# Performance work log

Measured on AMD Instinct MI355X. Metric: run time of the kernel, lower is better.

Reference implementation:

```python
import jax, jax.numpy as jnp
import numpy as np

N_NODES = 100000
N_EDGES = 1600000
VOCAB = 50000
EMB = 128
HID = 128
N_CLASSES = 10
N_GRAPHS = 512


def gcn_conv(x, src, dst, W, b, n_nodes):
    # PyG GCNConv: add self-loops, symmetric normalization D^-1/2 (A+I) D^-1/2, then linear.
    h = x @ W  # [N, H]
    loop = jnp.arange(n_nodes)
    s = jnp.concatenate([src, loop])
    d = jnp.concatenate([dst, loop])
    deg = jax.ops.segment_sum(jnp.ones_like(d, dtype=h.dtype), d, num_segments=n_nodes)
    dinv = jnp.where(deg > 0, jax.lax.rsqrt(deg), 0.0)
    norm = dinv[s] * dinv[d]  # [E+N]
    msg = h[s] * norm[:, None]  # gather + scale
    out = jax.ops.segment_sum(msg, d, num_segments=n_nodes)  # scatter-add
    return out + b


def setup_inputs() -> dict:
    key = jax.random.key(0)
    ks = jax.random.split(key, 10)
    x_idx = jax.random.randint(ks[0], (N_NODES,), 0, VOCAB)
    edge_index = jax.random.randint(ks[1], (2, N_EDGES), 0, N_NODES)
    batch = jnp.sort(jax.random.randint(ks[2], (N_NODES,), 0, N_GRAPHS))
    emb = jax.random.normal(ks[3], (VOCAB, EMB), dtype=jnp.float32)
    W1 = jax.random.normal(ks[4], (EMB, HID), dtype=jnp.float32) / np.sqrt(EMB)
    b1 = jnp.zeros((HID,), dtype=jnp.float32)
    W2 = jax.random.normal(ks[5], (HID, HID), dtype=jnp.float32) / np.sqrt(HID)
    b2 = jnp.zeros((HID,), dtype=jnp.float32)
    linW = jax.random.normal(ks[6], (HID, N_CLASSES), dtype=jnp.float32) / np.sqrt(HID)
    linb = jnp.zeros((N_CLASSES,), dtype=jnp.float32)
    return {"x_idx": x_idx, "edge_index": edge_index, "batch": batch,
            "emb": emb, "W1": W1, "b1": b1, "W2": W2, "b2": b2,
            "linW": linW, "linb": linb}


def reference(x_idx, edge_index, batch, emb, W1, b1, W2, b2, linW, linb):
    src, dst = edge_index[0], edge_index[1]
    x = emb[x_idx]  # embedding lookup [N, EMB]
    x = jax.nn.relu(gcn_conv(x, src, dst, W1, b1, N_NODES))
    x = jax.nn.relu(gcn_conv(x, src, dst, W2, b2, N_NODES))
    # global mean pool per graph
    sums = jax.ops.segment_sum(x, batch, num_segments=N_GRAPHS)  # [G, HID]
    cnts = jax.ops.segment_sum(jnp.ones((x.shape[0],), x.dtype), batch, num_segments=N_GRAPHS)
    pooled = sums / jnp.maximum(cnts, 1.0)[:, None]
    return pooled @ linW + linb  # [G, N_CLASSES]
```

## Files before the change

### kernel.cpp

```cpp
#include <hip/hip_runtime.h>
#include <hip/hip_bf16.h>

#define N_NODES   100000
#define N_EDGES   1600000
#define EMB       128
#define HID       128
#define N_CLASSES 10
#define N_GRAPHS  512
#define BUCKET_CAP 64

#define BIN_SHIFT 10
#define N_BINS    98
#define BIN_CAP   20480
#define EPB_A     4096

typedef unsigned int   uint;
typedef unsigned short ushort;
typedef __attribute__((ext_vector_type(8))) short bf16x8;
typedef __attribute__((ext_vector_type(4))) float f32x4;

#define MFMA_16x16x32(a, b, c) __builtin_amdgcn_mfma_f32_16x16x32_bf16((a), (b), (c), 0, 0, 0)

__device__ __forceinline__ ushort f2bf(float f) {
    uint u = __float_as_uint(f);
    return (ushort)((u + 0x7FFFu + ((u >> 16) & 1u)) >> 16);
}
__device__ __forceinline__ float bf2f(ushort h) {
    return __uint_as_float(((uint)h) << 16);
}

__device__ __forceinline__ void bf8_accum(uint4 q, float* acc) {
    acc[0] += __uint_as_float(q.x << 16);
    acc[1] += __uint_as_float(q.x & 0xFFFF0000u);
    acc[2] += __uint_as_float(q.y << 16);
    acc[3] += __uint_as_float(q.y & 0xFFFF0000u);
    acc[4] += __uint_as_float(q.z << 16);
    acc[5] += __uint_as_float(q.z & 0xFFFF0000u);
    acc[6] += __uint_as_float(q.w << 16);
    acc[7] += __uint_as_float(q.w & 0xFFFF0000u);
}

__global__ __launch_bounds__(256) void k_bin_edges(const int* __restrict__ src,
                                                   const int* __restrict__ dst,
                                                   int* __restrict__ bincur,
                                                   int2* __restrict__ binned) {
    __shared__ int lcnt[N_BINS];
    __shared__ int lbase[N_BINS];
    const int t = threadIdx.x;
    for (int b = t; b < N_BINS; b += 256) lcnt[b] = 0;
    __syncthreads();

    const int e0 = blockIdx.x * EPB_A;
    int s[16], d[16], slot[16];
    #pragma unroll
    for (int i = 0; i < 16; ++i) {
        int e = e0 + i * 256 + t;
        bool ok = e < N_EDGES;
        s[i] = ok ? src[e] : 0;
        d[i] = ok ? dst[e] : -1;
        slot[i] = ok ? atomicAdd(&lcnt[d[i] >> BIN_SHIFT], 1) : 0;
    }
    __syncthreads();
    for (int b = t; b < N_BINS; b += 256)
        lbase[b] = lcnt[b] ? atomicAdd(&bincur[b], lcnt[b]) : 0;
    __syncthreads();
    #pragma unroll
    for (int i = 0; i < 16; ++i) {
        if (d[i] >= 0) {
            int b = d[i] >> BIN_SHIFT;
            int pos = lbase[b] + slot[i];
            if (pos < BIN_CAP)
                binned[(size_t)b * BIN_CAP + pos] = make_int2(s[i], d[i]);
        }
    }
}

__global__ __launch_bounds__(1024) void k_bucket_from_bins(const int* __restrict__ bincur,
                                                           const int2* __restrict__ binned,
                                                           int* __restrict__ bucket,
                                                           int* __restrict__ deg,
                                                           float* __restrict__ dinv) {
    const int bin  = blockIdx.x;
    const int base = bin << BIN_SHIFT;
    const int nn   = min(1024, N_NODES - base);
    __shared__ int cnt[1024];
    const int t = threadIdx.x;
    cnt[t] = 0;
    __syncthreads();

    const int total = min(bincur[bin], BIN_CAP);
    const int2* bp = binned + (size_t)bin * BIN_CAP;
    for (int i = t; i < total; i += 1024) {
        int2 sd = bp[i];
        int slot = atomicAdd(&cnt[sd.y - base], 1);
        if (slot < BUCKET_CAP) bucket[(size_t)sd.y * BUCKET_CAP + slot] = sd.x;
    }
    __syncthreads();
    if (t < nn) {
        int c = cnt[t];
        deg[base + t]  = (c > BUCKET_CAP) ? BUCKET_CAP : c;
        dinv[base + t] = rsqrtf((float)(c + 1));
    }
}

template <bool USE_IDX, bool XBF>
__global__ __launch_bounds__(256) void k_gemm_mfma(const void* __restrict__ Xv,
                                                   const int* __restrict__ idx,
                                                   const float* __restrict__ W,
                                                   const float* __restrict__ dinv,
                                                   ushort* __restrict__ Ybf, int nrows) {
    __shared__ ushort Whi[16 * 128 * 8];
    __shared__ ushort Wlo[16 * 128 * 8];

    for (int p = threadIdx.x; p < 16 * 128; p += 256) {
        int koct = p >> 7, n = p & 127;
        bf16x8 hi, lo;
        #pragma unroll
        for (int j = 0; j < 8; ++j) {
            float w = W[(koct * 8 + j) * 128 + n];
            ushort h = f2bf(w);
            hi[j] = (short)h;
            lo[j] = (short)f2bf(w - bf2f(h));
        }
        reinterpret_cast<bf16x8*>(Whi)[p] = hi;
        reinterpret_cast<bf16x8*>(Wlo)[p] = lo;
    }
    __syncthreads();

    const int lane = threadIdx.x & 63;
    const int wid  = threadIdx.x >> 6;
    const int lm   = lane & 15;
    const int lk   = lane >> 4;

    const int wrow0 = blockIdx.x * 128 + wid * 32;
    if (wrow0 >= nrows) return;

    const float*  Xf = (const float*)Xv;
    const ushort* Xb = (const ushort*)Xv;

    size_t rowbase[2];
    bool rowok[2];
    #pragma unroll
    for (int m = 0; m < 2; ++m) {
        int row = wrow0 + m * 16 + lm;
        rowok[m] = row < nrows;
        int srcrow = rowok[m] ? (USE_IDX ? idx[row] : row) : 0;
        rowbase[m] = (size_t)srcrow * 128;
    }

    const bf16x8* WhiV = reinterpret_cast<const bf16x8*>(Whi);
    const bf16x8* WloV = reinterpret_cast<const bf16x8*>(Wlo);

    f32x4 acc[2][8];
    #pragma unroll
    for (int m = 0; m < 2; ++m)
        #pragma unroll
        for (int nt = 0; nt < 8; ++nt)
            acc[m][nt] = (f32x4){0.f, 0.f, 0.f, 0.f};

    if constexpr (XBF) {
        uint4 nb_[2];
        #pragma unroll
        for (int m = 0; m < 2; ++m)
            nb_[m] = rowok[m] ? *reinterpret_cast<const uint4*>(Xb + rowbase[m] + lk * 8)
                              : (uint4){0, 0, 0, 0};

        #pragma unroll 1
        for (int ks = 0; ks < 4; ++ks) {
            uint4 cb[2];
            #pragma unroll
            for (int m = 0; m < 2; ++m) cb[m] = nb_[m];
            if (ks < 3) {
                #pragma unroll
                for (int m = 0; m < 2; ++m)
                    nb_[m] = rowok[m] ? *reinterpret_cast<const uint4*>(Xb + rowbase[m] + (ks + 1) * 32 + lk * 8)
                                      : (uint4){0, 0, 0, 0};
            }
            bf16x8 ah[2];
            #pragma unroll
            for (int m = 0; m < 2; ++m) ah[m] = *reinterpret_cast<const bf16x8*>(&cb[m]);

            const int kbase = (ks * 4 + lk) * 128;
            #pragma unroll
            for (int nt = 0; nt < 8; ++nt) {
                bf16x8 bhi = WhiV[kbase + nt * 16 + lm];
                bf16x8 blo = WloV[kbase + nt * 16 + lm];
                #pragma unroll
                for (int m = 0; m < 2; ++m) {
                    acc[m][nt] = MFMA_16x16x32(ah[m], bhi, acc[m][nt]);
                    acc[m][nt] = MFMA_16x16x32(ah[m], blo, acc[m][nt]);
                }
            }
        }
    } else {
        float4 nx[2][2];
        #pragma unroll
        for (int m = 0; m < 2; ++m) {
            nx[m][0] = rowok[m] ? reinterpret_cast<const float4*>(Xf + rowbase[m] + lk * 8)[0] : (float4){0, 0, 0, 0};
            nx[m][1] = rowok[m] ? reinterpret_cast<const float4*>(Xf + rowbase[m] + lk * 8 + 4)[0] : (float4){0, 0, 0, 0};
        }

        #pragma unroll 1
        for (int ks = 0; ks < 4; ++ks) {
            float4 cx[2][2];
            #pragma unroll
            for (int m = 0; m < 2; ++m) { cx[m][0] = nx[m][0]; cx[m][1] = nx[m][1]; }
            if (ks < 3) {
                #pragma unroll
                for (int m = 0; m < 2; ++m) {
                    const float* base = Xf + rowbase[m] + (ks + 1) * 32 + lk * 8;
                    nx[m][0] = rowok[m] ? reinterpret_cast<const float4*>(base)[0] : (float4){0, 0, 0, 0};
                    nx[m][1] = rowok[m] ? reinterpret_cast<const float4*>(base + 4)[0] : (float4){0, 0, 0, 0};
                }
            }

            bf16x8 ahi[2], alo[2];
            #pragma unroll
            for (int m = 0; m < 2; ++m) {
                float xs[8] = {cx[m][0].x, cx[m][0].y, cx[m][0].z, cx[m][0].w,
                               cx[m][1].x, cx[m][1].y, cx[m][1].z, cx[m][1].w};
                #pragma unroll
                for (int j = 0; j < 8; ++j) {
                    uint u = __float_as_uint(xs[j]);
                    ushort h = (ushort)(u >> 16);
                    ahi[m][j] = (short)h;
                    float rem = xs[j] - bf2f(h);
                    alo[m][j] = (short)(__float_as_uint(rem) >> 16);
                }
            }

            const int kbase = (ks * 4 + lk) * 128;
            #pragma unroll
            for (int nt = 0; nt < 8; ++nt) {
                bf16x8 bhi = WhiV[kbase + nt * 16 + lm];
                bf16x8 blo = WloV[kbase + nt * 16 + lm];
                #pragma unroll
                for (int m = 0; m < 2; ++m) {
                    acc[m][nt] = MFMA_16x16x32(ahi[m], bhi, acc[m][nt]);
                    acc[m][nt] = MFMA_16x16x32(alo[m], bhi, acc[m][nt]);
                    acc[m][nt] = MFMA_16x16x32(ahi[m], blo, acc[m][nt]);
                }
            }
        }
    }

    #pragma unroll
    for (int m = 0; m < 2; ++m) {
        #pragma unroll
        for (int rg = 0; rg < 4; ++rg) {
            int row = wrow0 + m * 16 + lk * 4 + rg;
            if (row < nrows) {
                float dv = dinv[row];
                ushort* orow = Ybf + (size_t)row * 128 + lm;
                #pragma unroll
                for (int nt = 0; nt < 8; ++nt)
                    orow[nt * 16] = f2bf(acc[m][nt][rg] * dv);
            }
        }
    }
}

__global__ __launch_bounds__(256) void k_aggregate(const ushort* __restrict__ Ybf,
                                                   const int* __restrict__ deg,
                                                   const int* __restrict__ bucket,
                                                   const float* __restrict__ dinv,
                                                   const float* __restrict__ bias,
                                                   ushort* __restrict__ Abf) {
    int v = (blockIdx.x * 256 + threadIdx.x) >> 6;
    if (v >= N_NODES) return;
    int lane = threadIdx.x & 63;
    int oct = lane & 15;
    int par = lane >> 4;
    int n = deg[v];
    const int* nb = bucket + (size_t)v * BUCKET_CAP;
    const uint4* Yb = reinterpret_cast<const uint4*>(Ybf);

    float acc[8] = {0.f, 0.f, 0.f, 0.f, 0.f, 0.f, 0.f, 0.f};
    if (par == 0) bf8_accum(Yb[(size_t)v * 16 + oct], acc);

    int j = par;
    for (; j + 12 < n; j += 16) {
        uint4 q0 = Yb[(size_t)nb[j]      * 16 + oct];
        uint4 q1 = Yb[(size_t)nb[j + 4]  * 16 + oct];
        uint4 q2 = Yb[(size_t)nb[j + 8]  * 16 + oct];
        uint4 q3 = Yb[(size_t)nb[j + 12] * 16 + oct];
        bf8_accum(q0, acc); bf8_accum(q1, acc);
        bf8_accum(q2, acc); bf8_accum(q3, acc);
    }
    for (; j < n; j += 4) {
        bf8_accum(Yb[(size_t)nb[j] * 16 + oct], acc);
    }

    #pragma unroll
    for (int i = 0; i < 8; ++i) {
        acc[i] += __shfl_xor(acc[i], 16);
        acc[i] += __shfl_xor(acc[i], 32);
    }

    if (par == 0) {
        float dv = dinv[v];
        float4 b0 = reinterpret_cast<const float4*>(bias)[oct * 2];
        float4 b1 = reinterpret_cast<const float4*>(bias)[oct * 2 + 1];
        float r[8];
        r[0] = fmaxf(acc[0] * dv + b0.x, 0.f);
        r[1] = fmaxf(acc[1] * dv + b0.y, 0.f);
        r[2] = fmaxf(acc[2] * dv + b0.z, 0.f);
        r[3] = fmaxf(acc[3] * dv + b0.w, 0.f);
        r[4] = fmaxf(acc[4] * dv + b1.x, 0.f);
        r[5] = fmaxf(acc[5] * dv + b1.y, 0.f);
        r[6] = fmaxf(acc[6] * dv + b1.z, 0.f);
        r[7] = fmaxf(acc[7] * dv + b1.w, 0.f);
        uint4 o;
        o.x = (uint)f2bf(r[0]) | ((uint)f2bf(r[1]) << 16);
        o.y = (uint)f2bf(r[2]) | ((uint)f2bf(r[3]) << 16);
        o.z = (uint)f2bf(r[4]) | ((uint)f2bf(r[5]) << 16);
        o.w = (uint)f2bf(r[6]) | ((uint)f2bf(r[7]) << 16);
        reinterpret_cast<uint4*>(Abf)[(size_t)v * 16 + oct] = o;
    }
}

__global__ __launch_bounds__(256) void k_pool(const ushort* __restrict__ Abf,
                                              const int* __restrict__ batch,
                                              float* __restrict__ psum,
                                              float* __restrict__ pcnt) {
    int g = blockIdx.x;
    int lo = 0, hi = N_NODES;
    while (lo < hi) { int mid = (lo + hi) >> 1; if (batch[mid] < g) lo = mid + 1; else hi = mid; }
    int start = lo;
    hi = N_NODES;
    while (lo < hi) { int mid = (lo + hi) >> 1; if (batch[mid] < g + 1) lo = mid + 1; else hi = mid; }
    int end = lo;

    int t  = threadIdx.x;
    int cp = t & 63;
    int h  = t >> 6;
    float a0 = 0.f, a1 = 0.f;
    for (int n = start + h; n < end; n += 4) {
        uint q = *reinterpret_cast<const uint*>(Abf + (size_t)n * 128 + cp * 2);
        a0 += __uint_as_float(q << 16);
        a1 += __uint_as_float(q & 0xFFFF0000u);
    }
    __shared__ float sh[4][128];
    sh[h][cp * 2]     = a0;
    sh[h][cp * 2 + 1] = a1;
    __syncthreads();
    if (t < 128) {
        float s = sh[0][t] + sh[1][t] + sh[2][t] + sh[3][t];
        psum[g * 128 + t] = s;
        if (t == 0) pcnt[g] = (float)(end - start);
    }
}

__global__ __launch_bounds__(256) void k_final(const float* __restrict__ psum,
                                               const float* __restrict__ pcnt,
                                               const float* __restrict__ linW,
                                               const float* __restrict__ linb,
                                               float* __restrict__ out) {
    int tid = blockIdx.x * 256 + threadIdx.x;
    if (tid >= N_GRAPHS * N_CLASSES) return;
    int g = tid / N_CLASSES, c = tid % N_CLASSES;
    float acc = 0.f;
    #pragma unroll 8
    for (int k = 0; k < HID; ++k) acc += psum[g * 128 + k] * linW[k * N_CLASSES + c];
    float cnt = fmaxf(pcnt[g], 1.0f);
    out[tid] = acc / cnt + linb[c];
}

extern "C" void kernel_launch(void* const* d_in, const int* in_sizes, int n_in,
                              void* d_out, int out_size, void* d_ws, size_t ws_size,
                              hipStream_t stream) {
    const int*   x_idx = (const int*)d_in[0];
    const int*   eidx  = (const int*)d_in[1];
    const int*   batch = (const int*)d_in[2];
    const float* emb   = (const float*)d_in[3];
    const float* W1    = (const float*)d_in[4];
    const float* b1    = (const float*)d_in[5];
    const float* W2    = (const float*)d_in[6];
    const float* b2    = (const float*)d_in[7];
    const float* linW  = (const float*)d_in[8];
    const float* linb  = (const float*)d_in[9];
    float* out = (float*)d_out;

    const int* src = eidx;
    const int* dst = eidx + N_EDGES;

    char* w = (char*)d_ws;
    ushort* Abf    = (ushort*)w; w += (size_t)N_NODES * 128 * 2;
    ushort* Ybf    = (ushort*)w; w += (size_t)N_NODES * 128 * 2;
    float*  psum   = (float*)w;  w += (size_t)N_GRAPHS * 128 * 4;
    float*  pcnt   = (float*)w;  w += (size_t)N_GRAPHS * 4;
    float*  dinv   = (float*)w;  w += (size_t)N_NODES * 4;
    int*    deg    = (int*)w;    w += (size_t)N_NODES * 4;
    int*    bucket = (int*)w;    w += (size_t)N_NODES * BUCKET_CAP * 4;
    int*    bincur = (int*)w;    w += (size_t)N_BINS * 4;
    w = (char*)(((size_t)w + 15) & ~(size_t)15);
    int2*   binned = (int2*)w;   w += (size_t)N_BINS * BIN_CAP * 8;

    const int TPB = 256;
    const int gW  = (N_NODES * 64 + TPB - 1) / TPB;
    const int gG  = (N_NODES + 127) / 128;
    const int gA  = (N_EDGES + EPB_A - 1) / EPB_A;

    hipMemsetAsync(bincur, 0, (size_t)N_BINS * 4, stream);
    k_bin_edges<<<gA, TPB, 0, stream>>>(src, dst, bincur, binned);
    k_bucket_from_bins<<<N_BINS, 1024, 0, stream>>>(bincur, binned, bucket, deg, dinv);

    k_gemm_mfma<true, false><<<gG, TPB, 0, stream>>>(emb, x_idx, W1, dinv, Ybf, N_NODES);
    k_aggregate<<<gW, TPB, 0, stream>>>(Ybf, deg, bucket, dinv, b1, Abf);

    k_gemm_mfma<false, true><<<gG, TPB, 0, stream>>>(Abf, nullptr, W2, dinv, Ybf, N_NODES);
    k_aggregate<<<gW, TPB, 0, stream>>>(Ybf, deg, bucket, dinv, b2, Abf);

    k_pool<<<N_GRAPHS, TPB, 0, stream>>>(Abf, batch, psum, pcnt);
    k_final<<<(N_GRAPHS * N_CLASSES + TPB - 1) / TPB, TPB, 0, stream>>>(psum, pcnt, linW, linb, out);
}
```

Before: 260.7 us.

## Fuse edge binning with first GEMM and move source-degree scaling into aggregation

The GEMMs no longer depend on dinv, so the first GEMM is launched in the same grid as the edge-binning kernel and the two run concurrently. Source-side normalization moves into the aggregation gather as a per-neighbor dinv load and FMA. Binned edges are also packed into one 32-bit word (17-bit source, 10-bit local destination), halving that intermediate buffer. The cost is an extra random dinv gather per edge in both aggregation passes, plus a larger fused kernel whose two block types need different resources.

```diff
diff --git a/kernel.cpp b/kernel.cpp
--- a/kernel.cpp
+++ b/kernel.cpp
@@ -13,6 +13,8 @@
 #define N_BINS    98
 #define BIN_CAP   20480
 #define EPB_A     4096
+#define GA_BLOCKS ((N_EDGES + EPB_A - 1) / EPB_A)
+#define GG_BLOCKS ((N_NODES + 127) / 128)
 
 typedef unsigned int   uint;
 typedef unsigned short ushort;
@@ -29,28 +31,28 @@
     return __uint_as_float(((uint)h) << 16);
 }
 
-__device__ __forceinline__ void bf8_accum(uint4 q, float* acc) {
-    acc[0] += __uint_as_float(q.x << 16);
-    acc[1] += __uint_as_float(q.x & 0xFFFF0000u);
-    acc[2] += __uint_as_float(q.y << 16);
-    acc[3] += __uint_as_float(q.y & 0xFFFF0000u);
-    acc[4] += __uint_as_float(q.z << 16);
-    acc[5] += __uint_as_float(q.z & 0xFFFF0000u);
-    acc[6] += __uint_as_float(q.w << 16);
-    acc[7] += __uint_as_float(q.w & 0xFFFF0000u);
-}
-
-__global__ __launch_bounds__(256) void k_bin_edges(const int* __restrict__ src,
-                                                   const int* __restrict__ dst,
-                                                   int* __restrict__ bincur,
-                                                   int2* __restrict__ binned) {
+__device__ __forceinline__ void bf8_fma(uint4 q, float s, float* acc) {
+    acc[0] = fmaf(__uint_as_float(q.x << 16),          s, acc[0]);
+    acc[1] = fmaf(__uint_as_float(q.x & 0xFFFF0000u),  s, acc[1]);
+    acc[2] = fmaf(__uint_as_float(q.y << 16),          s, acc[2]);
+    acc[3] = fmaf(__uint_as_float(q.y & 0xFFFF0000u),  s, acc[3]);
+    acc[4] = fmaf(__uint_as_float(q.z << 16),          s, acc[4]);
+    acc[5] = fmaf(__uint_as_float(q.z & 0xFFFF0000u),  s, acc[5]);
+    acc[6] = fmaf(__uint_as_float(q.w << 16),          s, acc[6]);
+    acc[7] = fmaf(__uint_as_float(q.w & 0xFFFF0000u),  s, acc[7]);
+}
+
+__device__ void bin_edges_dev(int bid, const int* __restrict__ src,
+                              const int* __restrict__ dst,
+                              int* __restrict__ bincur,
+                              int* __restrict__ binned) {
     __shared__ int lcnt[N_BINS];
     __shared__ int lbase[N_BINS];
     const int t = threadIdx.x;
     for (int b = t; b < N_BINS; b += 256) lcnt[b] = 0;
     __syncthreads();
 
-    const int e0 = blockIdx.x * EPB_A;
+    const int e0 = bid * EPB_A;
     int s[16], d[16], slot[16];
     #pragma unroll
     for (int i = 0; i < 16; ++i) {
@@ -70,13 +72,188 @@
             int b = d[i] >> BIN_SHIFT;
             int pos = lbase[b] + slot[i];
             if (pos < BIN_CAP)
-                binned[(size_t)b * BIN_CAP + pos] = make_int2(s[i], d[i]);
-        }
-    }
+                binned[(size_t)b * BIN_CAP + pos] = s[i] | ((d[i] & 1023) << 17);
+        }
+    }
+}
+
+template <bool USE_IDX, bool XBF>
+__device__ void gemm_dev(int bid, const void* __restrict__ Xv,
+                         const int* __restrict__ idx,
+                         const float* __restrict__ W,
+                         ushort* __restrict__ Ybf, int nrows) {
+    __shared__ ushort Whi[16 * 128 * 8];
+    __shared__ ushort Wlo[16 * 128 * 8];
+
+    for (int p = threadIdx.x; p < 16 * 128; p += 256) {
+        int koct = p >> 7, n = p & 127;
+        bf16x8 hi, lo;
+        #pragma unroll
+        for (int j = 0; j < 8; ++j) {
+            float w = W[(koct * 8 + j) * 128 + n];
+            ushort h = f2bf(w);
+            hi[j] = (short)h;
+            lo[j] = (short)f2bf(w - bf2f(h));
+        }
+        reinterpret_cast<bf16x8*>(Whi)[p] = hi;
+        reinterpret_cast<bf16x8*>(Wlo)[p] = lo;
+    }
+    __syncthreads();
+
+    const int lane = threadIdx.x & 63;
+    const int wid  = threadIdx.x >> 6;
+    const int lm   = lane & 15;
+    const int lk   = lane >> 4;
+
+    const int wrow0 = bid * 128 + wid * 32;
+    if (wrow0 >= nrows) return;
+
+    const float*  Xf = (const float*)Xv;
+    const ushort* Xb = (const ushort*)Xv;
+
+    size_t rowbase[2];
+    bool rowok[2];
+    #pragma unroll
+    for (int m = 0; m < 2; ++m) {
+        int row = wrow0 + m * 16 + lm;
+        rowok[m] = row < nrows;
+        int srcrow = rowok[m] ? (USE_IDX ? idx[row] : row) : 0;
+        rowbase[m] = (size_t)srcrow * 128;
+    }
+
+    const bf16x8* WhiV = reinterpret_cast<const bf16x8*>(Whi);
+    const bf16x8* WloV = reinterpret_cast<const bf16x8*>(Wlo);
+
+    f32x4 acc[2][8];
+    #pragma unroll
+    for (int m = 0; m < 2; ++m)
+        #pragma unroll
+        for (int nt = 0; nt < 8; ++nt)
+            acc[m][nt] = (f32x4){0.f, 0.f, 0.f, 0.f};
+
+    if constexpr (XBF) {
+        uint4 nb_[2];
+        #pragma unroll
+        for (int m = 0; m < 2; ++m)
+            nb_[m] = rowok[m] ? *reinterpret_cast<const uint4*>(Xb + rowbase[m] + lk * 8)
+                              : (uint4){0, 0, 0, 0};
+
+        #pragma unroll 1
+        for (int ks = 0; ks < 4; ++ks) {
+            uint4 cb[2];
+            #pragma unroll
+            for (int m = 0; m < 2; ++m) cb[m] = nb_[m];
+            if (ks < 3) {
+                #pragma unroll
+                for (int m = 0; m < 2; ++m)
+                    nb_[m] = rowok[m] ? *reinterpret_cast<const uint4*>(Xb + rowbase[m] + (ks + 1) * 32 + lk * 8)
+                                      : (uint4){0, 0, 0, 0};
+            }
+            bf16x8 ah[2];
+            #pragma unroll
+            for (int m = 0; m < 2; ++m) ah[m] = *reinterpret_cast<const bf16x8*>(&cb[m]);
+
+            const int kbase = (ks * 4 + lk) * 128;
+            #pragma unroll
+            for (int nt = 0; nt < 8; ++nt) {
+                bf16x8 bhi = WhiV[kbase + nt * 16 + lm];
+                bf16x8 blo = WloV[kbase + nt * 16 + lm];
+                #pragma unroll
+                for (int m = 0; m < 2; ++m) {
+                    acc[m][nt] = MFMA_16x16x32(ah[m], bhi, acc[m][nt]);
+                    acc[m][nt] = MFMA_16x16x32(ah[m], blo, acc[m][nt]);
+                }
+            }
+        }
+    } else {
+        float4 nx[2][2];
+        #pragma unroll
+        for (int m = 0; m < 2; ++m) {
+            nx[m][0] = rowok[m] ? reinterpret_cast<const float4*>(Xf + rowbase[m] + lk * 8)[0] : (float4){0, 0, 0, 0};
+            nx[m][1] = rowok[m] ? reinterpret_cast<const float4*>(Xf + rowbase[m] + lk * 8 + 4)[0] : (float4){0, 0, 0, 0};
+        }
+
+        #pragma unroll 1
+        for (int ks = 0; ks < 4; ++ks) {
+            float4 cx[2][2];
+            #pragma unroll
+            for (int m = 0; m < 2; ++m) { cx[m][0] = nx[m][0]; cx[m][1] = nx[m][1]; }
+            if (ks < 3) {
+                #pragma unroll
+                for (int m = 0; m < 2; ++m) {
+                    const float* base = Xf + rowbase[m] + (ks + 1) * 32 + lk * 8;
+                    nx[m][0] = rowok[m] ? reinterpret_cast<const float4*>(base)[0] : (float4){0, 0, 0, 0};
+                    nx[m][1] = rowok[m] ? reinterpret_cast<const float4*>(base + 4)[0] : (float4){0, 0, 0, 0};
+                }
+            }
+
+            bf16x8 ahi[2], alo[2];
+            #pragma unroll
+            for (int m = 0; m < 2; ++m) {
+                float xs[8] = {cx[m][0].x, cx[m][0].y, cx[m][0].z, cx[m][0].w,
+                               cx[m][1].x, cx[m][1].y, cx[m][1].z, cx[m][1].w};
+                #pragma unroll
+                for (int j = 0; j < 8; ++j) {
+                    uint u = __float_as_uint(xs[j]);
+                    ushort h = (ushort)(u >> 16);
+                    ahi[m][j] = (short)h;
+                    float rem = xs[j] - bf2f(h);
+                    alo[m][j] = (short)(__float_as_uint(rem) >> 16);
+                }
+            }
+
+            const int kbase = (ks * 4 + lk) * 128;
+            #pragma unroll
+            for (int nt = 0; nt < 8; ++nt) {
+                bf16x8 bhi = WhiV[kbase + nt * 16 + lm];
+                bf16x8 blo = WloV[kbase + nt * 16 + lm];
+                #pragma unroll
+                for (int m = 0; m < 2; ++m) {
+                    acc[m][nt] = MFMA_16x16x32(ahi[m], bhi, acc[m][nt]);
+                    acc[m][nt] = MFMA_16x16x32(alo[m], bhi, acc[m][nt]);
+                    acc[m][nt] = MFMA_16x16x32(ahi[m], blo, acc[m][nt]);
+                }
+            }
+        }
+    }
+
+    #pragma unroll
+    for (int m = 0; m < 2; ++m) {
+        #pragma unroll
+        for (int rg = 0; rg < 4; ++rg) {
+            int row = wrow0 + m * 16 + lk * 4 + rg;
+            if (row < nrows) {
+                ushort* orow = Ybf + (size_t)row * 128 + lm;
+                #pragma unroll
+                for (int nt = 0; nt < 8; ++nt)
+                    orow[nt * 16] = f2bf(acc[m][nt][rg]);
+            }
+        }
+    }
+}
+
+__global__ __launch_bounds__(256) void k_fused_bin_gemm1(const int* __restrict__ src,
+                                                         const int* __restrict__ dst,
+                                                         int* __restrict__ bincur,
+                                                         int* __restrict__ binned,
+                                                         const float* __restrict__ emb,
+                                                         const int* __restrict__ x_idx,
+                                                         const float* __restrict__ W1,
+                                                         ushort* __restrict__ Ybf) {
+    if (blockIdx.x < GA_BLOCKS)
+        bin_edges_dev(blockIdx.x, src, dst, bincur, binned);
+    else
+        gemm_dev<true, false>(blockIdx.x - GA_BLOCKS, emb, x_idx, W1, Ybf, N_NODES);
+}
+
+__global__ __launch_bounds__(256) void k_gemm2(const ushort* __restrict__ Abf,
+                                               const float* __restrict__ W2,
+                                               ushort* __restrict__ Ybf) {
+    gemm_dev<false, true>(blockIdx.x, Abf, nullptr, W2, Ybf, N_NODES);
 }
 
 __global__ __launch_bounds__(1024) void k_bucket_from_bins(const int* __restrict__ bincur,
-                                                           const int2* __restrict__ binned,
+                                                           const int* __restrict__ binned,
                                                            int* __restrict__ bucket,
                                                            int* __restrict__ deg,
                                                            float* __restrict__ dinv) {
@@ -89,174 +266,19 @@
     __syncthreads();
 
     const int total = min(bincur[bin], BIN_CAP);
-    const int2* bp = binned + (size_t)bin * BIN_CAP;
+    const int* bp = binned + (size_t)bin * BIN_CAP;
     for (int i = t; i < total; i += 1024) {
-        int2 sd = bp[i];
-        int slot = atomicAdd(&cnt[sd.y - base], 1);
-        if (slot < BUCKET_CAP) bucket[(size_t)sd.y * BUCKET_CAP + slot] = sd.x;
+        int wrd = bp[i];
+        int s  = wrd & 0x1FFFF;
+        int ld = wrd >> 17;
+        int slot = atomicAdd(&cnt[ld], 1);
+        if (slot < BUCKET_CAP) bucket[(size_t)(base + ld) * BUCKET_CAP + slot] = s;
     }
     __syncthreads();
     if (t < nn) {
         int c = cnt[t];
         deg[base + t]  = (c > BUCKET_CAP) ? BUCKET_CAP : c;
         dinv[base + t] = rsqrtf((float)(c + 1));
-    }
-}
-
-template <bool USE_IDX, bool XBF>
-__global__ __launch_bounds__(256) void k_gemm_mfma(const void* __restrict__ Xv,
-                                                   const int* __restrict__ idx,
-                                                   const float* __restrict__ W,
-                                                   const float* __restrict__ dinv,
-                                                   ushort* __restrict__ Ybf, int nrows) {
-    __shared__ ushort Whi[16 * 128 * 8];
-    __shared__ ushort Wlo[16 * 128 * 8];
-
-    for (int p = threadIdx.x; p < 16 * 128; p += 256) {
-        int koct = p >> 7, n = p & 127;
-        bf16x8 hi, lo;
-        #pragma unroll
-        for (int j = 0; j < 8; ++j) {
-            float w = W[(koct * 8 + j) * 128 + n];
-            ushort h = f2bf(w);
-            hi[j] = (short)h;
-            lo[j] = (short)f2bf(w - bf2f(h));
-        }
-        reinterpret_cast<bf16x8*>(Whi)[p] = hi;
-        reinterpret_cast<bf16x8*>(Wlo)[p] = lo;
-    }
-    __syncthreads();
-
-    const int lane = threadIdx.x & 63;
-    const int wid  = threadIdx.x >> 6;
-    const int lm   = lane & 15;
-    const int lk   = lane >> 4;
-
-    const int wrow0 = blockIdx.x * 128 + wid * 32;
-    if (wrow0 >= nrows) return;
-
-    const float*  Xf = (const float*)Xv;
-    const ushort* Xb = (const ushort*)Xv;
-
-    size_t rowbase[2];
-    bool rowok[2];
-    #pragma unroll
-    for (int m = 0; m < 2; ++m) {
-        int row = wrow0 + m * 16 + lm;
-        rowok[m] = row < nrows;
-        int srcrow = rowok[m] ? (USE_IDX ? idx[row] : row) : 0;
-        rowbase[m] = (size_t)srcrow * 128;
-    }
-
-    const bf16x8* WhiV = reinterpret_cast<const bf16x8*>(Whi);
-    const bf16x8* WloV = reinterpret_cast<const bf16x8*>(Wlo);
-
-    f32x4 acc[2][8];
-    #pragma unroll
-    for (int m = 0; m < 2; ++m)
-        #pragma unroll
-        for (int nt = 0; nt < 8; ++nt)
-            acc[m][nt] = (f32x4){0.f, 0.f, 0.f, 0.f};
-
-    if constexpr (XBF) {
-        uint4 nb_[2];
-        #pragma unroll
-        for (int m = 0; m < 2; ++m)
-            nb_[m] = rowok[m] ? *reinterpret_cast<const uint4*>(Xb + rowbase[m] + lk * 8)
-                              : (uint4){0, 0, 0, 0};
-
-        #pragma unroll 1
-        for (int ks = 0; ks < 4; ++ks) {
-            uint4 cb[2];
-            #pragma unroll
-            for (int m = 0; m < 2; ++m) cb[m] = nb_[m];
-            if (ks < 3) {
-                #pragma unroll
-                for (int m = 0; m < 2; ++m)
-                    nb_[m] = rowok[m] ? *reinterpret_cast<const uint4*>(Xb + rowbase[m] + (ks + 1) * 32 + lk * 8)
-                                      : (uint4){0, 0, 0, 0};
-            }
-            bf16x8 ah[2];
-            #pragma unroll
-            for (int m = 0; m < 2; ++m) ah[m] = *reinterpret_cast<const bf16x8*>(&cb[m]);
-
-            const int kbase = (ks * 4 + lk) * 128;
-            #pragma unroll
-            for (int nt = 0; nt < 8; ++nt) {
-                bf16x8 bhi = WhiV[kbase + nt * 16 + lm];
-                bf16x8 blo = WloV[kbase + nt * 16 + lm];
-                #pragma unroll
-                for (int m = 0; m < 2; ++m) {
-                    acc[m][nt] = MFMA_16x16x32(ah[m], bhi, acc[m][nt]);
-                    acc[m][nt] = MFMA_16x16x32(ah[m], blo, acc[m][nt]);
-                }
-            }
-        }
-    } else {
-        float4 nx[2][2];
-        #pragma unroll
-        for (int m = 0; m < 2; ++m) {
-            nx[m][0] = rowok[m] ? reinterpret_cast<const float4*>(Xf + rowbase[m] + lk * 8)[0] : (float4){0, 0, 0, 0};
-            nx[m][1] = rowok[m] ? reinterpret_cast<const float4*>(Xf + rowbase[m] + lk * 8 + 4)[0] : (float4){0, 0, 0, 0};
-        }
-
-        #pragma unroll 1
-        for (int ks = 0; ks < 4; ++ks) {
-            float4 cx[2][2];
-            #pragma unroll
-            for (int m = 0; m < 2; ++m) { cx[m][0] = nx[m][0]; cx[m][1] = nx[m][1]; }
-            if (ks < 3) {
-                #pragma unroll
-                for (int m = 0; m < 2; ++m) {
-                    const float* base = Xf + rowbase[m] + (ks + 1) * 32 + lk * 8;
-                    nx[m][0] = rowok[m] ? reinterpret_cast<const float4*>(base)[0] : (float4){0, 0, 0, 0};
-                    nx[m][1] = rowok[m] ? reinterpret_cast<const float4*>(base + 4)[0] : (float4){0, 0, 0, 0};
-                }
-            }
-
-            bf16x8 ahi[2], alo[2];
-            #pragma unroll
-            for (int m = 0; m < 2; ++m) {
-                float xs[8] = {cx[m][0].x, cx[m][0].y, cx[m][0].z, cx[m][0].w,
-                               cx[m][1].x, cx[m][1].y, cx[m][1].z, cx[m][1].w};
-                #pragma unroll
-                for (int j = 0; j < 8; ++j) {
-                    uint u = __float_as_uint(xs[j]);
-                    ushort h = (ushort)(u >> 16);
-                    ahi[m][j] = (short)h;
-                    float rem = xs[j] - bf2f(h);
-                    alo[m][j] = (short)(__float_as_uint(rem) >> 16);
-                }
-            }
-
-            const int kbase = (ks * 4 + lk) * 128;
-            #pragma unroll
-            for (int nt = 0; nt < 8; ++nt) {
-                bf16x8 bhi = WhiV[kbase + nt * 16 + lm];
-                bf16x8 blo = WloV[kbase + nt * 16 + lm];
-                #pragma unroll
-                for (int m = 0; m < 2; ++m) {
-                    acc[m][nt] = MFMA_16x16x32(ahi[m], bhi, acc[m][nt]);
-                    acc[m][nt] = MFMA_16x16x32(alo[m], bhi, acc[m][nt]);
-                    acc[m][nt] = MFMA_16x16x32(ahi[m], blo, acc[m][nt]);
-                }
-            }
-        }
-    }
-
-    #pragma unroll
-    for (int m = 0; m < 2; ++m) {
-        #pragma unroll
-        for (int rg = 0; rg < 4; ++rg) {
-            int row = wrow0 + m * 16 + lk * 4 + rg;
-            if (row < nrows) {
-                float dv = dinv[row];
-                ushort* orow = Ybf + (size_t)row * 128 + lm;
-                #pragma unroll
-                for (int nt = 0; nt < 8; ++nt)
-                    orow[nt * 16] = f2bf(acc[m][nt][rg] * dv);
-            }
-        }
     }
 }
 
@@ -274,21 +296,25 @@
     int n = deg[v];
     const int* nb = bucket + (size_t)v * BUCKET_CAP;
     const uint4* Yb = reinterpret_cast<const uint4*>(Ybf);
+    const float dv = dinv[v];
 
     float acc[8] = {0.f, 0.f, 0.f, 0.f, 0.f, 0.f, 0.f, 0.f};
-    if (par == 0) bf8_accum(Yb[(size_t)v * 16 + oct], acc);
+    if (par == 0) bf8_fma(Yb[(size_t)v * 16 + oct], dv, acc);
 
     int j = par;
     for (; j + 12 < n; j += 16) {
-        uint4 q0 = Yb[(size_t)nb[j]      * 16 + oct];
-        uint4 q1 = Yb[(size_t)nb[j + 4]  * 16 + oct];
-        uint4 q2 = Yb[(size_t)nb[j + 8]  * 16 + oct];
-        uint4 q3 = Yb[(size_t)nb[j + 12] * 16 + oct];
-        bf8_accum(q0, acc); bf8_accum(q1, acc);
-        bf8_accum(q2, acc); bf8_accum(q3, acc);
+        int s0 = nb[j], s1 = nb[j + 4], s2 = nb[j + 8], s3 = nb[j + 12];
+        float d0 = dinv[s0], d1 = dinv[s1], d2 = dinv[s2], d3 = dinv[s3];
+        uint4 q0 = Yb[(size_t)s0 * 16 + oct];
+        uint4 q1 = Yb[(size_t)s1 * 16 + oct];
+        uint4 q2 = Yb[(size_t)s2 * 16 + oct];
+        uint4 q3 = Yb[(size_t)s3 * 16 + oct];
+        bf8_fma(q0, d0, acc); bf8_fma(q1, d1, acc);
+        bf8_fma(q2, d2, acc); bf8_fma(q3, d3, acc);
     }
     for (; j < n; j += 4) {
-        bf8_accum(Yb[(size_t)nb[j] * 16 + oct], acc);
+        int s0 = nb[j];
+        bf8_fma(Yb[(size_t)s0 * 16 + oct], dinv[s0], acc);
     }
 
     #pragma unroll
@@ -298,7 +324,6 @@
     }
 
     if (par == 0) {
-        float dv = dinv[v];
         float4 b0 = reinterpret_cast<const float4*>(bias)[oct * 2];
         float4 b1 = reinterpret_cast<const float4*>(bias)[oct * 2 + 1];
         float r[8];
@@ -394,21 +419,19 @@
     int*    bucket = (int*)w;    w += (size_t)N_NODES * BUCKET_CAP * 4;
     int*    bincur = (int*)w;    w += (size_t)N_BINS * 4;
     w = (char*)(((size_t)w + 15) & ~(size_t)15);
-    int2*   binned = (int2*)w;   w += (size_t)N_BINS * BIN_CAP * 8;
+    int*    binned = (int*)w;    w += (size_t)N_BINS * BIN_CAP * 4;
 
     const int TPB = 256;
     const int gW  = (N_NODES * 64 + TPB - 1) / TPB;
-    const int gG  = (N_NODES + 127) / 128;
-    const int gA  = (N_EDGES + EPB_A - 1) / EPB_A;
 
     hipMemsetAsync(bincur, 0, (size_t)N_BINS * 4, stream);
-    k_bin_edges<<<gA, TPB, 0, stream>>>(src, dst, bincur, binned);
+    k_fused_bin_gemm1<<<GA_BLOCKS + GG_BLOCKS, TPB, 0, stream>>>(src, dst, bincur, binned,
+                                                                 emb, x_idx, W1, Ybf);
     k_bucket_from_bins<<<N_BINS, 1024, 0, stream>>>(bincur, binned, bucket, deg, dinv);
 
-    k_gemm_mfma<true, false><<<gG, TPB, 0, stream>>>(emb, x_idx, W1, dinv, Ybf, N_NODES);
     k_aggregate<<<gW, TPB, 0, stream>>>(Ybf, deg, bucket, dinv, b1, Abf);
 
-    k_gemm_mfma<false, true><<<gG, TPB, 0, stream>>>(Abf, nullptr, W2, dinv, Ybf, N_NODES);
+    k_gemm2<<<GG_BLOCKS, TPB, 0, stream>>>(Abf, W2, Ybf);
     k_aggregate<<<gW, TPB, 0, stream>>>(Ybf, deg, bucket, dinv, b2, Abf);
 
     k_pool<<<N_GRAPHS, TPB, 0, stream>>>(Abf, batch, psum, pcnt);
```

After: 246.4 us. -5.5%, faster.
